# Performance work log

Measured on AMD Instinct MI355X. Metric: run time of the kernel, lower is better.

Reference implementation:

```python
import jax, jax.numpy as jnp
import numpy as np


def setup_inputs() -> dict:
    key = jax.random.key(0)
    ks = jax.random.split(key, 8)
    N, C, T, V = 32, 64, 256, 25
    OUT, INTER, S = 64, 16, 3
    W_SCALE = 0.05  # keep complex softmax exp() well-conditioned
    return {
        "x_real": jax.random.normal(ks[0], (N, C, T, V), jnp.float32),
        "x_imag": jax.random.normal(ks[1], (N, C, T, V), jnp.float32),
        "A": jax.random.uniform(ks[2], (S, V, V), jnp.float32),
        "PA": jax.random.normal(ks[3], (S, V, V), jnp.float32) * 1e-3,
        "Wa": jax.random.normal(ks[4], (S, 2 * INTER, 2 * C), jnp.float32) * W_SCALE,
        "ba": jnp.zeros((S, 2 * INTER), jnp.float32),
        "Wb": jax.random.normal(ks[5], (S, 2 * INTER, 2 * C), jnp.float32) * W_SCALE,
        "bb": jnp.zeros((S, 2 * INTER), jnp.float32),
        "Wd": jax.random.normal(ks[6], (S, 2 * OUT, 2 * C), jnp.float32) * W_SCALE,
        "bd": jnp.zeros((S, 2 * OUT), jnp.float32),
        "bn_weight": jnp.ones((OUT,), jnp.float32),
        "bn_bias": jnp.zeros((OUT,), jnp.float32),
    }


def _cconv1x1(z, W, b):
    # C_Conv2d with k=1: 1x1 conv over concat(real, imag) channels.
    zc = jnp.concatenate([z.real, z.imag], axis=1)          # [N, 2*Cin, T, V]
    o = jnp.einsum("oc,nctv->notv", W, zc) + b[None, :, None, None]
    h = W.shape[0] // 2
    return jax.lax.complex(o[:, :h], o[:, h:])              # [N, Cout, T, V] complex


def _forward(x_real, x_imag, A, PA, Wa, ba, Wb, bb, Wd, bd, bn_weight, bn_bias):
    x = jax.lax.complex(x_real, x_imag)                     # [N, C, T, V]
    N, C, T, V = x.shape
    inter = Wa.shape[1] // 2
    Afull = A + PA                                          # [3, V, V] real
    X2 = x.reshape(N, C * T, V)
    y = None
    for i in range(A.shape[0]):
        A1 = _cconv1x1(x, Wa[i], ba[i])                     # [N, inter, T, V]
        A1 = A1.transpose(0, 3, 1, 2).reshape(N, V, inter * T)
        A2 = _cconv1x1(x, Wb[i], bb[i]).reshape(N, inter * T, V)
        S = jnp.matmul(A1, A2) / (inter * T)                # [N, V, V] complex
        # complex softmax over dim=1 (no max-subtraction, faithful to C_softmax)
        ez = jnp.exp(S)
        S = ez / jnp.sum(ez, axis=1, keepdims=True)
        S = S + Afull[i]
        z = jnp.matmul(X2, S).reshape(N, C, T, V)
        z = _cconv1x1(z, Wd[i], bd[i])                      # [N, OUT, T, V]
        y = z if y is None else y + z
    # C_BatchNorm2d on complex input: complex mean, real variance = E|y-mu|^2
    mu = jnp.mean(y, axis=(0, 2, 3))                        # [OUT] complex
    var = jnp.mean(jnp.abs(y - mu[None, :, None, None]) ** 2, axis=(0, 2, 3))
    yn = (y - mu[None, :, None, None]) / jnp.sqrt(var + 1e-5)[None, :, None, None]
    yn = yn * bn_weight[None, :, None, None] + bn_bias[None, :, None, None]
    yn = yn + x  # down = identity (in_channels == out_channels)
    return jnp.stack([yn.real, yn.imag])                    # [2, N, OUT, T, V] real


def reference(x_real, x_imag, A, PA, Wa, ba, Wb, bb, Wd, bd, bn_weight, bn_bias):
    return _forward(x_real, x_imag, A, PA, Wa, ba, Wb, bb, Wd, bd, bn_weight, bn_bias)
```

## Files before the change

### kernel.cpp

```cpp
#include <hip/hip_runtime.h>
#include <hip/hip_bf16.h>
#include <stdint.h>

#define NN 32
#define CC 64
#define TTOT 256
#define VV 25
#define NS 3
constexpr int TV  = TTOT * VV;
constexpr int CTV = CC * TV;
constexpr size_t PLANE = (size_t)NN * CTV;

typedef unsigned short ushort_t;
using short8 = __attribute__((ext_vector_type(8))) short;
using f32x4  = __attribute__((ext_vector_type(4))) float;

static __device__ __forceinline__ ushort_t f2bf(float f) {
  __hip_bfloat16 h = __float2bfloat16(f);
  return reinterpret_cast<ushort_t&>(h);
}
static __device__ __forceinline__ float bf2f(ushort_t h) {
  union { uint32_t u; float f; } v; v.u = ((uint32_t)h) << 16;
  return v.f;
}
static __device__ __forceinline__ int SWZ(int row, int k) {
  return ((row << 7) + k) ^ ((row & 7) << 3);
}
static __device__ __forceinline__ f32x4 mfma16(short8 a, short8 b, f32x4 c) {
  return __builtin_amdgcn_mfma_f32_16x16x32_bf16(a, b, c, 0, 0, 0);
}
static __device__ __forceinline__ short8 negbf8(short8 x) {
  short8 r;
#pragma unroll
  for (int j = 0; j < 8; ++j) r[j] = x[j] ^ (short)0x8000;
  return r;
}

__global__ __launch_bounds__(256) void k0_wfrag(
    const float* __restrict__ Wd, const float* __restrict__ Wa,
    const float* __restrict__ Wb, ushort_t* __restrict__ wfrag,
    ushort_t* __restrict__ wab)
{
  const int i = blockIdx.x;
  for (int e = threadIdx.x; e < 16384; e += 256) {
    int ot = e >> 11, m = (e >> 9) & 3, l = (e >> 3) & 63, j = e & 7;
    int r  = ot * 16 + (l & 15);
    int c = m * 16 + ((l >> 4) << 2) + (j >> 1), comp = j & 1;
    wfrag[(size_t)i * 16384 + e] = f2bf(Wd[(size_t)i * 16384 + r * 128 + comp * 64 + c]);
  }
  for (int e = threadIdx.x; e < 8192; e += 256) {
    int mt = e >> 11, ks = (e >> 9) & 3, l = (e >> 3) & 63, j = e & 7;
    int r  = mt * 16 + (l & 15);
    int kp = ks * 32 + ((l >> 4) << 3) + j;
    float v = (r < 32) ? Wa[((size_t)i * 32 + r) * 128 + kp]
                       : Wb[((size_t)i * 32 + (r - 32)) * 128 + kp];
    wab[(size_t)i * 8192 + e] = f2bf(v);
  }
}

__global__ __launch_bounds__(256) void k1_spart(
    const float* __restrict__ xr, const float* __restrict__ xi,
    const ushort_t* __restrict__ wab, const float* __restrict__ ba,
    const float* __restrict__ bb, float* __restrict__ Spart)
{
  const int tc = blockIdx.x, n = blockIdx.y;
  const int tid = threadIdx.x, lane = tid & 63, wv = tid >> 6;
  const int r16 = lane & 15, gw = lane >> 4;
  __shared__ alignas(16) ushort_t zc[128 * 128];
  __shared__ alignas(16) ushort_t Ga[32 * 128];
  __shared__ alignas(16) ushort_t Gb[32 * 128];

  for (int e4 = tid; e4 < 128 * 25; e4 += 256) {
    int c = e4 / 25, q = e4 % 25;
    const float* src = (c < 64) ? xr : xi;
    float4 w = *(const float4*)&src[(size_t)n * CTV + (c & 63) * TV + tc * 100 + q * 4];
#pragma unroll
    for (int jj = 0; jj < 4; ++jj) {
      int g = q * 4 + jj, t = g / 25, v = g - t * 25;
      zc[SWZ(t * 32 + v, c)] = f2bf(((const float*)&w)[jj]);
    }
  }
  for (int e = tid; e < 28 * 128; e += 256) {
    int r7 = e >> 7, c = e & 127;
    int t = r7 / 7, vv = 25 + r7 % 7;
    zc[SWZ(t * 32 + vv, c)] = 0;
  }

  const int mu = wv >> 1, nv = wv & 1;

  for (int i = 0; i < NS; ++i) {
    __syncthreads();

    {
      short8 afr[4];
#pragma unroll
      for (int ks = 0; ks < 4; ++ks)
        afr[ks] = *(const short8*)&wab[((((size_t)i * 4 + wv) * 4 + ks) * 64 + lane) * 8];
      float bias[4];
#pragma unroll
      for (int j = 0; j < 4; ++j) {
        int row = wv * 16 + gw * 4 + j;
        bias[j] = (row < 32) ? ba[i * 32 + row] : bb[i * 32 + (row - 32)];
      }
      ushort_t* gbuf = (wv < 2) ? Ga : Gb;
      const int half = (wv & 1) * 64;
      for (int nt = 0; nt < 8; ++nt) {
        f32x4 acc = {0.f, 0.f, 0.f, 0.f};
        const int brow = nt * 16 + r16;
#pragma unroll
        for (int ks = 0; ks < 4; ++ks) {
          short8 bfr = *(const short8*)&zc[SWZ(brow, ks * 32 + gw * 8)];
          acc = mfma16(afr[ks], bfr, acc);
        }
        int pos2 = nt * 16 + r16;
        int t = pos2 >> 5, v = pos2 & 31;
        int k0w = half + t * 16 + gw * 4;
        uint32_t w0 = (uint32_t)f2bf(acc[0] + bias[0]) | ((uint32_t)f2bf(acc[1] + bias[1]) << 16);
        uint32_t w1 = (uint32_t)f2bf(acc[2] + bias[2]) | ((uint32_t)f2bf(acc[3] + bias[3]) << 16);
        uint2 pk; pk.x = w0; pk.y = w1;
        *(uint2*)&gbuf[SWZ(v, k0w)] = pk;
      }
    }
    __syncthreads();

    {
      const int urow = mu * 16 + r16;
      const int vrow = nv * 16 + r16;
      f32x4 Prr = {0.f,0.f,0.f,0.f}, Pii = {0.f,0.f,0.f,0.f};
      f32x4 Pri = {0.f,0.f,0.f,0.f}, Pir = {0.f,0.f,0.f,0.f};
#pragma unroll
      for (int ks = 0; ks < 2; ++ks) {
        int ko = ks * 32 + gw * 8;
        short8 arF = *(const short8*)&Ga[SWZ(urow, ko)];
        short8 aiF = *(const short8*)&Ga[SWZ(urow, 64 + ko)];
        short8 brF = *(const short8*)&Gb[SWZ(vrow, ko)];
        short8 biF = *(const short8*)&Gb[SWZ(vrow, 64 + ko)];
        Prr = mfma16(arF, brF, Prr);
        Pii = mfma16(aiF, biF, Pii);
        Pri = mfma16(arF, biF, Pri);
        Pir = mfma16(aiF, brF, Pir);
      }
#pragma unroll
      for (int j = 0; j < 4; ++j) {
        int u = mu * 16 + gw * 4 + j;
        int v = nv * 16 + r16;
        if (u < VV && v < VV) {
          size_t idx = ((((size_t)i * NN + n) * 64 + tc) * 625 + u * 25 + v) * 2;
          Spart[idx]     = Prr[j] - Pii[j];
          Spart[idx + 1] = Pri[j] + Pir[j];
        }
      }
    }
  }
}

__global__ __launch_bounds__(256) void k2_softmax(
    const float* __restrict__ Spart, const float* __restrict__ Aw,
    const float* __restrict__ PA, ushort_t* __restrict__ sfrag)
{
  const int i = blockIdx.x, n = blockIdx.y, tid = threadIdx.x;
  __shared__ float ez[625 * 2];
  __shared__ float den[25 * 2];
  for (int e = tid; e < 625; e += 256) {
    float sr = 0.f, si = 0.f;
    const float* p = Spart + (((size_t)i * NN + n) * 64 * 625 + e) * 2;
    for (int tcb = 0; tcb < 64; ++tcb) { sr += p[0]; si += p[1]; p += 625 * 2; }
    sr *= (1.f / 4096.f); si *= (1.f / 4096.f);
    float m = expf(sr);
    ez[e * 2] = m * cosf(si);
    ez[e * 2 + 1] = m * sinf(si);
  }
  __syncthreads();
  if (tid < 25) {
    float dr = 0.f, di = 0.f;
    for (int u = 0; u < 25; ++u) { dr += ez[(u * 25 + tid) * 2]; di += ez[(u * 25 + tid) * 2 + 1]; }
    float inv = 1.f / (dr * dr + di * di);
    den[tid * 2] = dr * inv; den[tid * 2 + 1] = -di * inv;
  }
  __syncthreads();
  for (int e = tid; e < 625; e += 256) {
    int v = e % 25;
    float er = ez[e * 2], ei = ez[e * 2 + 1];
    float dr = den[v * 2], di = den[v * 2 + 1];
    float outr = er * dr - ei * di + Aw[i * 625 + e] + PA[i * 625 + e];
    float outi = er * di + ei * dr;
    ez[e * 2] = outr; ez[e * 2 + 1] = outi;
  }
  __syncthreads();
  for (int e = tid; e < 512; e += 256) {
    int l = e & 63, nt = (e >> 6) & 1, m = e >> 7;
    int u0 = (l >> 4) << 3, v = nt * 16 + (l & 15);
    short8 pk;
#pragma unroll
    for (int j = 0; j < 8; ++j) {
      int u = u0 + j;
      float val = 0.f;
      if (u < VV && v < VV) {
        float sr_ = ez[(u * 25 + v) * 2], si_ = ez[(u * 25 + v) * 2 + 1];
        float base = (m < 2) ? sr_ : si_;
        if (m & 1) { float hi = bf2f(f2bf(base)); val = base - hi; }
        else val = base;
      }
      pk[j] = (short)f2bf(val);
    }
    *(short8*)&sfrag[((size_t)(i * NN + n) * 512 + e) * 8] = pk;
  }
}

__global__ __launch_bounds__(256) void k3_y(
    const float* __restrict__ xr, const float* __restrict__ xi,
    const ushort_t* __restrict__ sfrag, const ushort_t* __restrict__ wfrag,
    const float* __restrict__ bd, float* __restrict__ out,
    float* __restrict__ bnpart)
{
  const int tq = blockIdx.x, n = blockIdx.y;
  const int tid = threadIdx.x, lane = tid & 63, wv = tid >> 6;
  const int r16 = lane & 15, gw = lane >> 4;
  __shared__ alignas(16) ushort_t smem[16384];
  __shared__ float stats[4][128][2];

  for (int e4 = tid; e4 < 128 * 25; e4 += 256) {
    int c = e4 / 25, q = e4 % 25;
    const float* src = (c < 64) ? xr : xi;
    float4 w = *(const float4*)&src[(size_t)n * CTV + (c & 63) * TV + tq * 100 + q * 4];
#pragma unroll
    for (int jj = 0; jj < 4; ++jj) {
      int g = q * 4 + jj, t = g / 25, u = g - t * 25;
      smem[SWZ(c, t * 32 + u)] = f2bf(((const float*)&w)[jj]);
    }
  }
  for (int e = tid; e < 128 * 28; e += 256) {
    int c = e / 28, r = e % 28;
    int t = r / 7, u = 25 + r % 7;
    smem[SWZ(c, t * 32 + u)] = 0;
  }
  __syncthreads();

  const int kx = wv * 32 + gw * 8;
  short8 axr[4], axi[4];
#pragma unroll
  for (int tile = 0; tile < 4; ++tile) {
    axr[tile] = *(const short8*)&smem[SWZ(tile * 16 + r16, kx)];
    axi[tile] = *(const short8*)&smem[SWZ(64 + tile * 16 + r16, kx)];
  }
  __syncthreads();

  f32x4 acc[8][2];
#pragma unroll
  for (int a = 0; a < 8; ++a) { acc[a][0] = {0.f,0.f,0.f,0.f}; acc[a][1] = {0.f,0.f,0.f,0.f}; }

#pragma unroll 1
  for (int i = 0; i < NS; ++i) {
    {
      const ushort_t* wsrc = wfrag + (size_t)i * 16384;
      short8 tmp[8];
#pragma unroll
      for (int q = 0; q < 8; ++q)
        tmp[q] = *(const short8*)&wsrc[q * 2048 + tid * 8];
#pragma unroll
      for (int q = 0; q < 8; ++q)
        *(short8*)&smem[q * 2048 + tid * 8] = tmp[q];
    }
    const ushort_t* sb = sfrag + (size_t)(i * NN + n) * 4096;
    short8 sf[4][2];
#pragma unroll
    for (int m = 0; m < 4; ++m)
#pragma unroll
      for (int nt = 0; nt < 2; ++nt)
        sf[m][nt] = *(const short8*)&sb[((m * 2 + nt) * 64 + lane) * 8];
    __syncthreads();

    short8 sn0[2], sn1[2];
#pragma unroll
    for (int nt = 0; nt < 2; ++nt) { sn0[nt] = negbf8(sf[2][nt]); sn1[nt] = negbf8(sf[3][nt]); }

    short8 bp[4][2];
#pragma unroll
    for (int tile = 0; tile < 4; ++tile) {
#pragma unroll
      for (int nt = 0; nt < 2; ++nt) {
        f32x4 zr = {0.f,0.f,0.f,0.f}, zi = {0.f,0.f,0.f,0.f};
        zr = mfma16(axr[tile], sf[0][nt], zr);
        zr = mfma16(axr[tile], sf[1][nt], zr);
        zr = mfma16(axi[tile], sn0[nt], zr);
        zr = mfma16(axi[tile], sn1[nt], zr);
        zi = mfma16(axr[tile], sf[2][nt], zi);
        zi = mfma16(axr[tile], sf[3][nt], zi);
        zi = mfma16(axi[tile], sf[0][nt], zi);
        zi = mfma16(axi[tile], sf[1][nt], zi);
        short8 pk;
#pragma unroll
        for (int j = 0; j < 4; ++j) {
          pk[2 * j]     = (short)f2bf(zr[j]);
          pk[2 * j + 1] = (short)f2bf(zi[j]);
        }
        bp[tile][nt] = pk;
      }
    }

#pragma unroll
    for (int ot = 0; ot < 8; ++ot) {
#pragma unroll
      for (int m = 0; m < 4; ++m) {
        short8 a = *(const short8*)&smem[(((ot * 4 + m) * 64) + lane) * 8];
        acc[ot][0] = mfma16(a, bp[m][0], acc[ot][0]);
        acc[ot][1] = mfma16(a, bp[m][1], acc[ot][1]);
      }
    }
    __syncthreads();
  }

  const int t = tq * 4 + wv;
#pragma unroll
  for (int ot = 0; ot < 8; ++ot) {
#pragma unroll
    for (int j = 0; j < 4; ++j) {
      int row = ot * 16 + gw * 4 + j;
      float bias = bd[row] + bd[128 + row] + bd[256 + row];
      float s = 0.f, q = 0.f;
#pragma unroll
      for (int nt = 0; nt < 2; ++nt) {
        int v = nt * 16 + r16;
        float val = acc[ot][nt][j] + bias;
        if (v < VV) {
          out[(size_t)(row >> 6) * PLANE + (size_t)n * CTV + (row & 63) * TV + t * VV + v] = val;
          s += val; q += val * val;
        }
      }
#pragma unroll
      for (int d = 1; d < 16; d <<= 1) { s += __shfl_xor(s, d); q += __shfl_xor(q, d); }
      if (r16 == 0) { stats[wv][row][0] = s; stats[wv][row][1] = q; }
    }
  }
  __syncthreads();
  if (tid < 128) {
    float s = stats[0][tid][0] + stats[1][tid][0] + stats[2][tid][0] + stats[3][tid][0];
    float q = stats[0][tid][1] + stats[1][tid][1] + stats[2][tid][1] + stats[3][tid][1];
    size_t b = (size_t)n * 64 + tq;
    bnpart[(b * 128 + tid) * 2]     = s;
    bnpart[(b * 128 + tid) * 2 + 1] = q;
  }
}

__global__ __launch_bounds__(256) void k4_stats(
    const float* __restrict__ bnpart, const float* __restrict__ bnw,
    const float* __restrict__ bnb, float* __restrict__ coeff)
{
  const int o = blockIdx.x, tid = threadIdx.x;
  float sr = 0.f, qr = 0.f, si = 0.f, qi = 0.f;
  for (int b = tid; b < 2048; b += 256) {
    const float* p = bnpart + ((size_t)b * 128 + o) * 2;
    sr += p[0]; qr += p[1];
    const float* p2 = bnpart + ((size_t)b * 128 + 64 + o) * 2;
    si += p2[0]; qi += p2[1];
  }
#pragma unroll
  for (int d = 1; d < 64; d <<= 1) {
    sr += __shfl_xor(sr, d); qr += __shfl_xor(qr, d);
    si += __shfl_xor(si, d); qi += __shfl_xor(qi, d);
  }
  __shared__ float red[4][4];
  int lane = tid & 63, wv = tid >> 6;
  if (lane == 0) { red[wv][0] = sr; red[wv][1] = qr; red[wv][2] = si; red[wv][3] = qi; }
  __syncthreads();
  if (tid == 0) {
    sr = red[0][0] + red[1][0] + red[2][0] + red[3][0];
    qr = red[0][1] + red[1][1] + red[2][1] + red[3][1];
    si = red[0][2] + red[1][2] + red[2][2] + red[3][2];
    qi = red[0][3] + red[1][3] + red[2][3] + red[3][3];
    const float invM = 1.f / (float)((size_t)NN * TTOT * VV);
    float mur = sr * invM, mui = si * invM;
    float var = (qr + qi) * invM - mur * mur - mui * mui;
    float inv = rsqrtf(var + 1e-5f);
    coeff[o * 4 + 0] = mur; coeff[o * 4 + 1] = mui;
    coeff[o * 4 + 2] = inv * bnw[o]; coeff[o * 4 + 3] = bnb[o];
  }
}

__global__ __launch_bounds__(256) void k5_norm(
    const float* __restrict__ xr, const float* __restrict__ xi,
    const float* __restrict__ coeff, float* __restrict__ out)
{
  size_t idx0 = ((size_t)blockIdx.x * 256 + threadIdx.x) * 4;
  size_t stride = (size_t)gridDim.x * 256 * 4;
  for (size_t e = idx0; e < PLANE; e += stride) {
    int o = (int)((e / TV) & 63);
    float4 cf = *(const float4*)&coeff[o * 4];
    float4 yr = *(float4*)&out[e];
    float4 yi = *(float4*)&out[PLANE + e];
    float4 vr = *(const float4*)&xr[e];
    float4 vi = *(const float4*)&xi[e];
    yr.x = (yr.x - cf.x) * cf.z + cf.w + vr.x;
    yr.y = (yr.y - cf.x) * cf.z + cf.w + vr.y;
    yr.z = (yr.z - cf.x) * cf.z + cf.w + vr.z;
    yr.w = (yr.w - cf.x) * cf.z + cf.w + vr.w;
    yi.x = (yi.x - cf.y) * cf.z + vi.x;
    yi.y = (yi.y - cf.y) * cf.z + vi.y;
    yi.z = (yi.z - cf.y) * cf.z + vi.z;
    yi.w = (yi.w - cf.y) * cf.z + vi.w;
    *(float4*)&out[e] = yr;
    *(float4*)&out[PLANE + e] = yi;
  }
}

extern "C" void kernel_launch(void* const* d_in, const int* in_sizes, int n_in,
                              void* d_out, int out_size, void* d_ws, size_t ws_size,
                              hipStream_t stream) {
  const float* xr  = (const float*)d_in[0];
  const float* xi  = (const float*)d_in[1];
  const float* Aw  = (const float*)d_in[2];
  const float* PA  = (const float*)d_in[3];
  const float* Wa  = (const float*)d_in[4];
  const float* ba  = (const float*)d_in[5];
  const float* Wb  = (const float*)d_in[6];
  const float* bb  = (const float*)d_in[7];
  const float* Wd  = (const float*)d_in[8];
  const float* bd  = (const float*)d_in[9];
  const float* bnw = (const float*)d_in[10];
  const float* bnb = (const float*)d_in[11];
  float* out = (float*)d_out;
  float* ws = (float*)d_ws;

  float*    Spart  = ws;
  float*    bnpart = ws;
  ushort_t* sfrag  = (ushort_t*)(ws + 7680000);
  ushort_t* wfrag  = (ushort_t*)(ws + 7876608);
  ushort_t* wab    = (ushort_t*)(ws + 7901184);
  float*    coeff  = ws + 7913472;

  k0_wfrag<<<NS, 256, 0, stream>>>(Wd, Wa, Wb, wfrag, wab);
  k1_spart<<<dim3(64, NN), 256, 0, stream>>>(xr, xi, wab, ba, bb, Spart);
  k2_softmax<<<dim3(NS, NN), 256, 0, stream>>>(Spart, Aw, PA, sfrag);
  k3_y<<<dim3(64, NN), 256, 0, stream>>>(xr, xi, sfrag, wfrag, bd, out, bnpart);
  k4_stats<<<64, 256, 0, stream>>>(bnpart, bnw, bnb, coeff);
  k5_norm<<<6400, 256, 0, stream>>>(xr, xi, coeff, out);
}
```

Before: 246.4 us.

## Widen k3 blocks to 512 threads, preload all three Wd fragments into LDS

Each k3 block now has 8 waves and covers 8 timesteps instead of 4, so half as many blocks are launched. All three subset weight fragments are staged into a 96KB LDS buffer once, which removes the per-subset reload and the barriers inside the loop. S fragments for the next subset are prefetched into registers while the current one computes. The larger LDS footprint and register pressure (launch_bounds 512,2) may limit occupancy. The BN partial count in k4 is halved to match.

```diff
diff --git a/kernel.cpp b/kernel.cpp
--- a/kernel.cpp
+++ b/kernel.cpp
@@ -207,7 +207,7 @@
   }
 }
 
-__global__ __launch_bounds__(256) void k3_y(
+__global__ __launch_bounds__(512, 2) void k3_y(
     const float* __restrict__ xr, const float* __restrict__ xi,
     const ushort_t* __restrict__ sfrag, const ushort_t* __restrict__ wfrag,
     const float* __restrict__ bd, float* __restrict__ out,
@@ -216,32 +216,47 @@
   const int tq = blockIdx.x, n = blockIdx.y;
   const int tid = threadIdx.x, lane = tid & 63, wv = tid >> 6;
   const int r16 = lane & 15, gw = lane >> 4;
-  __shared__ alignas(16) ushort_t smem[16384];
-  __shared__ float stats[4][128][2];
-
-  for (int e4 = tid; e4 < 128 * 25; e4 += 256) {
-    int c = e4 / 25, q = e4 % 25;
-    const float* src = (c < 64) ? xr : xi;
-    float4 w = *(const float4*)&src[(size_t)n * CTV + (c & 63) * TV + tq * 100 + q * 4];
-#pragma unroll
-    for (int jj = 0; jj < 4; ++jj) {
-      int g = q * 4 + jj, t = g / 25, u = g - t * 25;
-      smem[SWZ(c, t * 32 + u)] = f2bf(((const float*)&w)[jj]);
-    }
-  }
-  for (int e = tid; e < 128 * 28; e += 256) {
-    int c = e / 28, r = e % 28;
-    int t = r / 7, u = 25 + r % 7;
-    smem[SWZ(c, t * 32 + u)] = 0;
-  }
-  __syncthreads();
-
-  const int kx = wv * 32 + gw * 8;
+  __shared__ alignas(16) ushort_t wlds[49152];
+  __shared__ float stats[8][128][2];
+
+  {
+    ushort_t* xs = wlds;
+    for (int e4 = tid; e4 < 128 * 50; e4 += 512) {
+      int c = e4 / 50, q = e4 % 50;
+      const float* src = (c < 64) ? xr : xi;
+      float4 w = *(const float4*)&src[(size_t)n * CTV + (c & 63) * TV + tq * 200 + q * 4];
+#pragma unroll
+      for (int jj = 0; jj < 4; ++jj) {
+        int g = q * 4 + jj, t = g / 25, u = g - t * 25;
+        xs[(t >> 2) * 16384 + SWZ(c, (t & 3) * 32 + u)] = f2bf(((const float*)&w)[jj]);
+      }
+    }
+    for (int e = tid; e < 128 * 56; e += 512) {
+      int c = e / 56, r = e % 56;
+      int t = r / 7, u = 25 + r % 7;
+      xs[(t >> 2) * 16384 + SWZ(c, (t & 3) * 32 + u)] = 0;
+    }
+  }
+  __syncthreads();
+
+  const int tl = wv & 3, th = wv >> 2;
+  const int kx = tl * 32 + gw * 8;
   short8 axr[4], axi[4];
 #pragma unroll
   for (int tile = 0; tile < 4; ++tile) {
-    axr[tile] = *(const short8*)&smem[SWZ(tile * 16 + r16, kx)];
-    axi[tile] = *(const short8*)&smem[SWZ(64 + tile * 16 + r16, kx)];
+    axr[tile] = *(const short8*)&wlds[th * 16384 + SWZ(tile * 16 + r16, kx)];
+    axi[tile] = *(const short8*)&wlds[th * 16384 + SWZ(64 + tile * 16 + r16, kx)];
+  }
+  __syncthreads();
+
+  {
+    short8 tmp[12];
+#pragma unroll
+    for (int q = 0; q < 12; ++q)
+      tmp[q] = *(const short8*)&wfrag[(size_t)(q * 512 + tid) * 8];
+#pragma unroll
+    for (int q = 0; q < 12; ++q)
+      *(short8*)&wlds[(size_t)(q * 512 + tid) * 8] = tmp[q];
   }
   __syncthreads();
 
@@ -249,31 +264,18 @@
 #pragma unroll
   for (int a = 0; a < 8; ++a) { acc[a][0] = {0.f,0.f,0.f,0.f}; acc[a][1] = {0.f,0.f,0.f,0.f}; }
 
-#pragma unroll 1
-  for (int i = 0; i < NS; ++i) {
-    {
-      const ushort_t* wsrc = wfrag + (size_t)i * 16384;
-      short8 tmp[8];
-#pragma unroll
-      for (int q = 0; q < 8; ++q)
-        tmp[q] = *(const short8*)&wsrc[q * 2048 + tid * 8];
-#pragma unroll
-      for (int q = 0; q < 8; ++q)
-        *(short8*)&smem[q * 2048 + tid * 8] = tmp[q];
-    }
+  auto load_sf = [&](int i, short8 sf[4][2]) {
     const ushort_t* sb = sfrag + (size_t)(i * NN + n) * 4096;
-    short8 sf[4][2];
 #pragma unroll
     for (int m = 0; m < 4; ++m)
 #pragma unroll
       for (int nt = 0; nt < 2; ++nt)
         sf[m][nt] = *(const short8*)&sb[((m * 2 + nt) * 64 + lane) * 8];
-    __syncthreads();
-
+  };
+  auto compute_i = [&](int i, short8 sf[4][2]) {
     short8 sn0[2], sn1[2];
 #pragma unroll
     for (int nt = 0; nt < 2; ++nt) { sn0[nt] = negbf8(sf[2][nt]); sn1[nt] = negbf8(sf[3][nt]); }
-
     short8 bp[4][2];
 #pragma unroll
     for (int tile = 0; tile < 4; ++tile) {
@@ -297,20 +299,26 @@
         bp[tile][nt] = pk;
       }
     }
-
 #pragma unroll
     for (int ot = 0; ot < 8; ++ot) {
 #pragma unroll
       for (int m = 0; m < 4; ++m) {
-        short8 a = *(const short8*)&smem[(((ot * 4 + m) * 64) + lane) * 8];
+        short8 a = *(const short8*)&wlds[((size_t)i * 16384) + (size_t)((ot * 4 + m) * 64 + lane) * 8];
         acc[ot][0] = mfma16(a, bp[m][0], acc[ot][0]);
         acc[ot][1] = mfma16(a, bp[m][1], acc[ot][1]);
       }
     }
-    __syncthreads();
-  }
-
-  const int t = tq * 4 + wv;
+  };
+
+  short8 sfA[4][2], sfB[4][2];
+  load_sf(0, sfA);
+  load_sf(1, sfB);
+  compute_i(0, sfA);
+  load_sf(2, sfA);
+  compute_i(1, sfB);
+  compute_i(2, sfA);
+
+  const int t = tq * 8 + wv;
 #pragma unroll
   for (int ot = 0; ot < 8; ++ot) {
 #pragma unroll
@@ -334,9 +342,10 @@
   }
   __syncthreads();
   if (tid < 128) {
-    float s = stats[0][tid][0] + stats[1][tid][0] + stats[2][tid][0] + stats[3][tid][0];
-    float q = stats[0][tid][1] + stats[1][tid][1] + stats[2][tid][1] + stats[3][tid][1];
-    size_t b = (size_t)n * 64 + tq;
+    float s = 0.f, q = 0.f;
+#pragma unroll
+    for (int w = 0; w < 8; ++w) { s += stats[w][tid][0]; q += stats[w][tid][1]; }
+    size_t b = (size_t)n * 32 + tq;
     bnpart[(b * 128 + tid) * 2]     = s;
     bnpart[(b * 128 + tid) * 2 + 1] = q;
   }
@@ -348,7 +357,7 @@
 {
   const int o = blockIdx.x, tid = threadIdx.x;
   float sr = 0.f, qr = 0.f, si = 0.f, qi = 0.f;
-  for (int b = tid; b < 2048; b += 256) {
+  for (int b = tid; b < 1024; b += 256) {
     const float* p = bnpart + ((size_t)b * 128 + o) * 2;
     sr += p[0]; qr += p[1];
     const float* p2 = bnpart + ((size_t)b * 128 + 64 + o) * 2;
@@ -431,7 +440,7 @@
   k0_wfrag<<<NS, 256, 0, stream>>>(Wd, Wa, Wb, wfrag, wab);
   k1_spart<<<dim3(64, NN), 256, 0, stream>>>(xr, xi, wab, ba, bb, Spart);
   k2_softmax<<<dim3(NS, NN), 256, 0, stream>>>(Spart, Aw, PA, sfrag);
-  k3_y<<<dim3(64, NN), 256, 0, stream>>>(xr, xi, sfrag, wfrag, bd, out, bnpart);
+  k3_y<<<dim3(32, NN), 512, 0, stream>>>(xr, xi, sfrag, wfrag, bd, out, bnpart);
   k4_stats<<<64, 256, 0, stream>>>(bnpart, bnw, bnb, coeff);
   k5_norm<<<6400, 256, 0, stream>>>(xr, xi, coeff, out);
 }
```

Result: no change. 245.2 us (-0.5%).
